# Optimization experiments

Hardware: AMD Instinct MI355X
Metric: run time of the kernel (lower is better)

## Reference

```python
import jax, jax.numpy as jnp
import numpy as np

F_DIM = 1024
HEAD = 16
MLP_H = 4096
EPS = 1e-5


def _layernorm(x, g, b):
    mu = jnp.mean(x, axis=-1, keepdims=True)
    var = jnp.var(x, axis=-1, keepdims=True)
    return (x - mu) * jax.lax.rsqrt(var + EPS) * g + b


def setup_inputs() -> dict:
    key = jax.random.key(0)
    ks = jax.random.split(key, 16)
    B, T, F = 2, 2048, F_DIM
    s = 1.0 / np.sqrt(F)
    sm = 1.0 / np.sqrt(MLP_H)
    return {
        "x": jax.random.normal(ks[0], (B, T, F), jnp.float32),
        "ln1_g": jnp.ones((F,), jnp.float32),
        "ln1_b": jnp.zeros((F,), jnp.float32),
        "Wq": jax.random.normal(ks[1], (F, F), jnp.float32) * s,
        "bq": jnp.zeros((F,), jnp.float32),
        "Wk": jax.random.normal(ks[2], (F, F), jnp.float32) * s,
        "bk": jnp.zeros((F,), jnp.float32),
        "Wv": jax.random.normal(ks[3], (F, F), jnp.float32) * s,
        "bv": jnp.zeros((F,), jnp.float32),
        "Wo": jax.random.normal(ks[4], (F, F), jnp.float32) * s,
        "bo": jnp.zeros((F,), jnp.float32),
        "ln2_g": jnp.ones((F,), jnp.float32),
        "ln2_b": jnp.zeros((F,), jnp.float32),
        "W1": jax.random.normal(ks[5], (F, MLP_H), jnp.float32) * s,
        "b1": jnp.zeros((MLP_H,), jnp.float32),
        "W2": jax.random.normal(ks[6], (MLP_H, F), jnp.float32) * sm,
        "b2": jnp.zeros((F,), jnp.float32),
    }


def reference(x, ln1_g, ln1_b, Wq, bq, Wk, bk, Wv, bv, Wo, bo, ln2_g, ln2_b, W1, b1, W2, b2):
    B, T, F = x.shape
    H, Dh = HEAD, F // HEAD
    sqrt_d = jnp.asarray(F, x.dtype) ** 0.5  # NOTE: scale by sqrt(features), as in source

    h = _layernorm(x, ln1_g, ln1_b)
    Q = (h @ Wq + bq).reshape(B, T, H, Dh).transpose(0, 2, 1, 3)  # bhtd
    K = (h @ Wk + bk).reshape(B, T, H, Dh).transpose(0, 2, 1, 3)
    V = (h @ Wv + bv).reshape(B, T, H, Dh).transpose(0, 2, 1, 3)

    scores = jnp.einsum('bhif,bhjf->bhij', Q, K) / sqrt_d
    attn_map = jax.nn.softmax(scores, axis=-1)
    attn = jnp.einsum('bhij,bhjf->bihf', attn_map, V)  # [B,T,H,Dh]
    attn_out = attn.reshape(B, T, F) @ Wo + bo
    out = attn_out + x

    h2 = _layernorm(out, ln2_g, ln2_b)
    mlp = jax.nn.gelu(jax.nn.gelu(h2 @ W1 + b1, approximate=False) @ W2 + b2, approximate=False)
    return mlp + out
```

## Files before the change

### kernel.cpp

```cpp
#include <hip/hip_runtime.h>
#include <hip/hip_bf16.h>
#include <math.h>
#include <stdint.h>

typedef __attribute__((ext_vector_type(8))) __bf16 bf16x8;
typedef __attribute__((ext_vector_type(4))) float f32x4;

#define F_DIM 1024
#define MLP_HD 4096
#define HEADS 16
#define DH 64
#define B_SZ 2
#define T_SZ 2048
#define NROWS 4096
#define QKV_N 3072
#define LN_EPS 1e-5f

__device__ __forceinline__ void gload16(const void* g, void* l) {
    __builtin_amdgcn_global_load_lds(
        (const __attribute__((address_space(1))) uint32_t*)(uintptr_t)g,
        (__attribute__((address_space(3))) uint32_t*)(uintptr_t)l,
        16, 0, 0);
}

__global__ void transpose_cast(const float* __restrict__ in,
                               __hip_bfloat16* __restrict__ out,
                               int R, int C) {
    __shared__ float tile[32][33];
    int c0 = blockIdx.x * 32, r0 = blockIdx.y * 32;
    int tx = threadIdx.x, ty = threadIdx.y;
    #pragma unroll
    for (int i = 0; i < 32; i += 8)
        tile[ty + i][tx] = in[(size_t)(r0 + ty + i) * C + c0 + tx];
    __syncthreads();
    #pragma unroll
    for (int i = 0; i < 32; i += 8)
        out[(size_t)(c0 + ty + i) * R + r0 + tx] = __float2bfloat16(tile[tx][ty + i]);
}

__global__ void transpose_v(const __hip_bfloat16* __restrict__ QKV,
                            __hip_bfloat16* __restrict__ VT) {
    __shared__ __hip_bfloat16 tile[32][33];
    int dblk = blockIdx.y & 1, bh = blockIdx.y >> 1;
    int b = bh >> 4, h = bh & 15;
    int t0 = blockIdx.x * 32, d0 = dblk * 32;
    int tx = threadIdx.x, ty = threadIdx.y;
    #pragma unroll
    for (int i = 0; i < 32; i += 8)
        tile[ty + i][tx] = QKV[(size_t)(b * T_SZ + t0 + ty + i) * QKV_N + 2048 + h * DH + d0 + tx];
    __syncthreads();
    #pragma unroll
    for (int i = 0; i < 32; i += 8)
        VT[(size_t)(bh * DH + d0 + ty + i) * T_SZ + t0 + tx] = tile[tx][ty + i];
}

__global__ void concat_bias(const float* __restrict__ a, const float* __restrict__ b,
                            const float* __restrict__ c, float* __restrict__ o) {
    int i = blockIdx.x * 256 + threadIdx.x;
    o[i] = i < 1024 ? a[i] : (i < 2048 ? b[i - 1024] : c[i - 2048]);
}

__global__ void layernorm_bf16_k(const float* __restrict__ x,
                                 const float* __restrict__ g,
                                 const float* __restrict__ b,
                                 __hip_bfloat16* __restrict__ out) {
    int row = blockIdx.x;
    const float* xr = x + (size_t)row * F_DIM;
    int t = threadIdx.x;
    float4 v = ((const float4*)xr)[t];
    float s  = v.x + v.y + v.z + v.w;
    float s2 = v.x * v.x + v.y * v.y + v.z * v.z + v.w * v.w;
    #pragma unroll
    for (int off = 32; off >= 1; off >>= 1) {
        s  += __shfl_down(s, off);
        s2 += __shfl_down(s2, off);
    }
    __shared__ float rs_[4], rs2_[4];
    int wave = t >> 6, lane = t & 63;
    if (lane == 0) { rs_[wave] = s; rs2_[wave] = s2; }
    __syncthreads();
    float S  = rs_[0] + rs_[1] + rs_[2] + rs_[3];
    float S2 = rs2_[0] + rs2_[1] + rs2_[2] + rs2_[3];
    float mu  = S * (1.0f / F_DIM);
    float var = S2 * (1.0f / F_DIM) - mu * mu;
    float rstd = rsqrtf(var + LN_EPS);
    float4 gv = ((const float4*)g)[t];
    float4 bv = ((const float4*)b)[t];
    __hip_bfloat16* orow = out + (size_t)row * F_DIM;
    orow[t * 4 + 0] = __float2bfloat16((v.x - mu) * rstd * gv.x + bv.x);
    orow[t * 4 + 1] = __float2bfloat16((v.y - mu) * rstd * gv.y + bv.y);
    orow[t * 4 + 2] = __float2bfloat16((v.z - mu) * rstd * gv.z + bv.z);
    orow[t * 4 + 3] = __float2bfloat16((v.w - mu) * rstd * gv.w + bv.w);
}

__device__ __forceinline__ float gelu_exact(float x) {
    return 0.5f * x * (1.0f + erff(x * 0.70710678f));
}

#define LA_PTR(BUF, H) ((__hip_bfloat16*)(SMEM + ((BUF) * 2 + (H)) * 16384))
#define LB_PTR(BUF, H) ((__hip_bfloat16*)(SMEM + 65536 + ((BUF) * 2 + (H)) * 16384))

#define MFMA_QUAD(AF, BF, MB, NB)                                              \
  do {                                                                         \
    __builtin_amdgcn_s_barrier();                                              \
    asm volatile("s_waitcnt lgkmcnt(0)" ::: "memory");                         \
    __builtin_amdgcn_sched_barrier(0);                                         \
    __builtin_amdgcn_s_setprio(1);                                             \
    _Pragma("unroll") for (int ks = 0; ks < 2; ++ks)                           \
      _Pragma("unroll") for (int a_ = 0; a_ < 4; ++a_)                         \
        _Pragma("unroll") for (int b_ = 0; b_ < 2; ++b_)                       \
          acc[(MB) + a_][(NB) + b_] = __builtin_amdgcn_mfma_f32_16x16x32_bf16( \
              AF[a_][ks], BF[b_][ks], acc[(MB) + a_][(NB) + b_], 0, 0, 0);     \
    __builtin_amdgcn_s_setprio(0);                                             \
  } while (0)

#define LDA_FRAGS(DST, BUF, MQ)                                                \
  do {                                                                         \
    _Pragma("unroll") for (int a_ = 0; a_ < 4; ++a_)                           \
      _Pragma("unroll") for (int ks = 0; ks < 2; ++ks) {                       \
        int row_ = (MQ) * 64 + a_ * 16 + fr;                                   \
        int byt_ = row_ * 128 + ((ks * 64 + fq * 16) ^ ((row_ & 7) << 4));     \
        DST[a_][ks] = *(const bf16x8*)((const char*)LA_PTR(BUF, wm) + byt_);   \
      }                                                                        \
  } while (0)

#define LDB_FRAGS(DST, BUF, NQ)                                                \
  do {                                                                         \
    _Pragma("unroll") for (int b_ = 0; b_ < 2; ++b_)                           \
      _Pragma("unroll") for (int ks = 0; ks < 2; ++ks) {                       \
        int row_ = (wn & 1) * 64 + ((NQ) * 2 + b_) * 16 + fr;                  \
        int byt_ = row_ * 128 + ((ks * 64 + fq * 16) ^ ((row_ & 7) << 4));     \
        DST[b_][ks] = *(const bf16x8*)((const char*)LB_PTR(BUF, hb) + byt_);   \
      }                                                                        \
  } while (0)

#define STAGE_A(BUF, H, KT_)                                                   \
  do {                                                                         \
    _Pragma("unroll") for (int q_ = 0; q_ < 2; ++q_)                           \
      gload16(A + (size_t)(m0 + (H) * 128 + srow[q_]) * K +                    \
                  (k00 + (KT_) * 64 + scol[q_]),                               \
              LA_PTR(BUF, H) + q_ * 4096 + t * 8);                             \
  } while (0)

#define STAGE_B(BUF, H, KT_)                                                   \
  do {                                                                         \
    _Pragma("unroll") for (int q_ = 0; q_ < 2; ++q_)                           \
      gload16(BT + (size_t)(n0 + (H) * 128 + srow[q_]) * K +                   \
                   (k00 + (KT_) * 64 + scol[q_]),                              \
              LB_PTR(BUF, H) + q_ * 4096 + t * 8);                             \
  } while (0)

template <int EPI, int KLEN>
__global__ __launch_bounds__(512, 2) void gemm256(
    const __hip_bfloat16* __restrict__ A,
    const __hip_bfloat16* __restrict__ BT,
    const float* __restrict__ bias,
    void* __restrict__ Cout,
    int M, int N, int K) {
    __shared__ __align__(16) char SMEM[131072];

    int t = threadIdx.x;
    int w = t >> 6, lane = t & 63;
    int wm = w >> 2, wn = w & 3;
    int fr = lane & 15, fq = lane >> 4;
    int hb = wn >> 1;

    int gx = gridDim.x, gy = gridDim.y, gz = gridDim.z;
    int bid = blockIdx.x + gx * (blockIdx.y + gy * blockIdx.z);
    int nwg = gx * gy * gz;
    int qch = nwg >> 3;
    int logical = (bid & 7) * qch + (bid >> 3);
    int pp = gy * gz;
    int bx = logical / pp;
    int rr = logical % pp;
    int by = rr / gz;
    int bz = rr % gz;

    int m0 = by * 256, n0 = bx * 256;
    int k00 = bz * KLEN;

    int srow[2], scol[2];
    #pragma unroll
    for (int q = 0; q < 2; ++q) {
        int u = q * 8192 + t * 16;
        u ^= ((u >> 7) & 7) << 4;
        srow[q] = u >> 7;
        scol[q] = (u & 127) >> 1;
    }

    f32x4 acc[8][4] = {};
    bf16x8 aflo[4][2], afhi[4][2], bflo[2][2], bfhi[2][2];
    constexpr int KT = KLEN >> 6;

    STAGE_A(0, 0, 0); STAGE_A(0, 1, 0); STAGE_B(0, 0, 0); STAGE_B(0, 1, 0);
    STAGE_A(1, 0, 1); STAGE_A(1, 1, 1);
    asm volatile("s_waitcnt vmcnt(4)" ::: "memory");
    __builtin_amdgcn_s_barrier();

    for (int i = 0;; ++i) {
        int k1 = 2 * i + 1;
        int nx2 = (2 * i + 2) & (KT - 1), nx3 = (2 * i + 3) & (KT - 1);
        LDA_FRAGS(aflo, 0, 0);
        LDB_FRAGS(bflo, 0, 0);
        STAGE_B(1, 0, k1);
        MFMA_QUAD(aflo, bflo, 0, 0);
        __builtin_amdgcn_s_barrier();
        LDA_FRAGS(afhi, 0, 1);
        STAGE_B(1, 1, k1);
        MFMA_QUAD(afhi, bflo, 4, 0);
        __builtin_amdgcn_s_barrier();
        LDB_FRAGS(bfhi, 0, 1);
        STAGE_A(0, 0, nx2);
        MFMA_QUAD(afhi, bfhi, 4, 2);
        __builtin_amdgcn_s_barrier();
        STAGE_A(0, 1, nx2);
        MFMA_QUAD(aflo, bfhi, 0, 2);
        asm volatile("s_waitcnt vmcnt(4)" ::: "memory");
        __builtin_amdgcn_s_barrier();
        LDA_FRAGS(aflo, 1, 0);
        LDB_FRAGS(bflo, 1, 0);
        STAGE_B(0, 0, nx2);
        MFMA_QUAD(aflo, bflo, 0, 0);
        __builtin_amdgcn_s_barrier();
        LDA_FRAGS(afhi, 1, 1);
        STAGE_B(0, 1, nx2);
        MFMA_QUAD(afhi, bflo, 4, 0);
        __builtin_amdgcn_s_barrier();
        LDB_FRAGS(bfhi, 1, 1);
        STAGE_A(1, 0, nx3);
        MFMA_QUAD(afhi, bfhi, 4, 2);
        __builtin_amdgcn_s_barrier();
        STAGE_A(1, 1, nx3);
        MFMA_QUAD(aflo, bfhi, 0, 2);
        asm volatile("s_waitcnt vmcnt(4)" ::: "memory");
        __builtin_amdgcn_s_barrier();
        if (2 * i + 2 >= KT) break;
    }

    asm volatile("s_waitcnt vmcnt(0)" ::: "memory");
    __builtin_amdgcn_s_barrier();

    #pragma unroll
    for (int ni = 0; ni < 4; ++ni) {
        int col = wn * 64 + ni * 16 + fr;
        float bv = (EPI == 4) ? 0.f : bias[n0 + col];
        #pragma unroll
        for (int mi = 0; mi < 8; ++mi) {
            #pragma unroll
            for (int j = 0; j < 4; ++j) {
                int row = wm * 128 + mi * 16 + fq * 4 + j;
                float v = acc[mi][ni][j] + bv;
                if constexpr (EPI == 2) v = gelu_exact(v);
                int byt = row * 512 + ((col * 2) ^ ((row & 7) << 4));
                *(__hip_bfloat16*)(SMEM + byt) = __float2bfloat16(v);
            }
        }
    }
    __builtin_amdgcn_s_barrier();

    __hip_bfloat16* outc = (__hip_bfloat16*)Cout;
    if constexpr (EPI == 4) outc += (size_t)bz * ((size_t)M * N);
    #pragma unroll
    for (int p = 0; p < 16; ++p) {
        int row = p * 16 + (t >> 5);
        int chunk = t & 31;
        int byt = row * 512 + ((chunk * 16) ^ ((row & 7) << 4));
        bf16x8 vv = *(const bf16x8*)(SMEM + byt);
        *(bf16x8*)&outc[(size_t)(m0 + row) * N + n0 + chunk * 8] = vv;
    }
}

__global__ __launch_bounds__(256) void mlp2_reduce(
    const __hip_bfloat16* __restrict__ P,
    const float* __restrict__ b2,
    const float* __restrict__ res,
    float* __restrict__ out) {
    int i = (blockIdx.x * 256 + threadIdx.x) * 8;
    float s[8] = {};
    #pragma unroll
    for (int sk = 0; sk < 4; ++sk) {
        bf16x8 v = *(const bf16x8*)&P[(size_t)sk * ((size_t)NROWS * F_DIM) + i];
        #pragma unroll
        for (int u = 0; u < 8; ++u) s[u] += (float)v[u];
    }
    int col = i & (F_DIM - 1);
    #pragma unroll
    for (int u = 0; u < 8; ++u)
        out[i + u] = gelu_exact(s[u] + b2[col + u]) + res[i + u];
}

template <int EPI, int BM>
__global__ __launch_bounds__(256) void gemm_bt(
    const __hip_bfloat16* __restrict__ A,
    const __hip_bfloat16* __restrict__ BT,
    const float* __restrict__ bias,
    const float* __restrict__ res,
    void* __restrict__ Cout,
    int M, int N, int K) {
    constexpr int MI = BM / 32;
    constexpr int AQ = BM / 64;
    __shared__ __hip_bfloat16 As[2][BM * 32];
    __shared__ __hip_bfloat16 Bs[2][128 * 32];

    int t = threadIdx.x;
    int m0 = blockIdx.y * BM, n0 = blockIdx.x * 128;
    int w = t >> 6, lane = t & 63;
    int wr = (w >> 1) * (BM / 2), wc = (w & 1) * 64;
    int fr = lane & 15, fq = lane >> 4;

    int scol = (lane & 3) * 8;
    int srowA = w * (BM / 4) + (lane >> 2);
    int srowB = w * 32 + (lane >> 2);
    const __hip_bfloat16* Ag = A  + (size_t)(m0 + srowA) * K + scol;
    const __hip_bfloat16* Bg = BT + (size_t)(n0 + srowB) * K + scol;
    int lofsA = w * (BM / 4) * 32 + lane * 8;
    int lofsB = w * 1024 + lane * 8;

    f32x4 acc[MI][4] = {};
    int KT = K >> 5;
    int cur = 0;

    #pragma unroll
    for (int q = 0; q < AQ; ++q)
        gload16(Ag + (size_t)q * 16 * K, &As[0][lofsA + q * 512]);
    #pragma unroll
    for (int q = 0; q < 2; ++q)
        gload16(Bg + (size_t)q * 16 * K, &Bs[0][lofsB + q * 512]);
    __syncthreads();

    for (int kt = 0; kt < KT; ++kt) {
        if (kt + 1 < KT) {
            const __hip_bfloat16* An = Ag + (size_t)(kt + 1) * 32;
            const __hip_bfloat16* Bn = Bg + (size_t)(kt + 1) * 32;
            #pragma unroll
            for (int q = 0; q < AQ; ++q)
                gload16(An + (size_t)q * 16 * K, &As[cur ^ 1][lofsA + q * 512]);
            #pragma unroll
            for (int q = 0; q < 2; ++q)
                gload16(Bn + (size_t)q * 16 * K, &Bs[cur ^ 1][lofsB + q * 512]);
        }
        bf16x8 af[MI], bfr[4];
        #pragma unroll
        for (int mi = 0; mi < MI; ++mi)
            af[mi] = *(const bf16x8*)&As[cur][(wr + mi * 16 + fr) * 32 + fq * 8];
        #pragma unroll
        for (int ni = 0; ni < 4; ++ni)
            bfr[ni] = *(const bf16x8*)&Bs[cur][(wc + ni * 16 + fr) * 32 + fq * 8];
        #pragma unroll
        for (int mi = 0; mi < MI; ++mi)
            #pragma unroll
            for (int ni = 0; ni < 4; ++ni)
                acc[mi][ni] = __builtin_amdgcn_mfma_f32_16x16x32_bf16(
                    af[mi], bfr[ni], acc[mi][ni], 0, 0, 0);
        __syncthreads();
        cur ^= 1;
    }

    #pragma unroll
    for (int ni = 0; ni < 4; ++ni) {
        int col = n0 + wc + ni * 16 + fr;
        float bv = bias[col];
        #pragma unroll
        for (int mi = 0; mi < MI; ++mi) {
            #pragma unroll
            for (int j = 0; j < 4; ++j) {
                int row = m0 + wr + mi * 16 + fq * 4 + j;
                size_t idx = (size_t)row * N + col;
                float v = acc[mi][ni][j] + bv;
                if constexpr (EPI == 1) {
                    ((float*)Cout)[idx] = v + res[idx];
                } else {
                    ((__hip_bfloat16*)Cout)[idx] = __float2bfloat16(v);
                }
            }
        }
    }
}

__global__ __launch_bounds__(256) void attn_mfma(
    const __hip_bfloat16* __restrict__ QKV,
    const __hip_bfloat16* __restrict__ VT,
    __hip_bfloat16* __restrict__ O) {
    __shared__ __hip_bfloat16 Kt[2][64][72];
    __shared__ __hip_bfloat16 Vt[2][64][72];
    __shared__ __hip_bfloat16 Ps[4][32][72];

    int blk = blockIdx.x;
    int qb = blk & 15;
    int bh = blk >> 4;
    int b = bh >> 4, h = bh & 15;
    int t = threadIdx.x;
    int w = t >> 6, lane = t & 63;
    int fr = lane & 15, fq = lane >> 4;

    bf16x8 qf[2][2];
    #pragma unroll
    for (int mt = 0; mt < 2; ++mt)
        #pragma unroll
        for (int ks = 0; ks < 2; ++ks) {
            int qrow = qb * 128 + w * 32 + mt * 16 + fr;
            const __hip_bfloat16* src =
                QKV + (size_t)(b * T_SZ + qrow) * QKV_N + h * DH + ks * 32 + fq * 8;
            bf16x8 v = *(const bf16x8*)src;
            #pragma unroll
            for (int u = 0; u < 8; ++u) v[u] = (__bf16)((float)v[u] * 0.03125f);
            qf[mt][ks] = v;
        }

    f32x4 oacc[2][4] = {};
    float lsum[2][4] = {};

    int sr = t >> 2;
    int sc = (t & 3) * 16;
    const __hip_bfloat16* Kg = QKV + (size_t)(b * T_SZ + sr) * QKV_N + F_DIM + h * DH + sc;
    const __hip_bfloat16* Vg = VT + (size_t)(bh * DH + sr) * T_SZ + sc;

    bf16x8 kr0, kr1, vr0, vr1;
    {
        kr0 = *(const bf16x8*)Kg;       kr1 = *(const bf16x8*)(Kg + 8);
        vr0 = *(const bf16x8*)Vg;       vr1 = *(const bf16x8*)(Vg + 8);
        *(bf16x8*)&Kt[0][sr][sc]     = kr0;
        *(bf16x8*)&Kt[0][sr][sc + 8] = kr1;
        *(bf16x8*)&Vt[0][sr][sc]     = vr0;
        *(bf16x8*)&Vt[0][sr][sc + 8] = vr1;
    }
    __syncthreads();

    int cur = 0;
    for (int j0 = 0; j0 < T_SZ; j0 += 64) {
        bool more = (j0 + 64 < T_SZ);
        if (more) {
            const __hip_bfloat16* kg = Kg + (size_t)(j0 + 64) * QKV_N;
            kr0 = *(const bf16x8*)kg;  kr1 = *(const bf16x8*)(kg + 8);
            const __hip_bfloat16* vg = Vg + (j0 + 64);
            vr0 = *(const bf16x8*)vg;  vr1 = *(const bf16x8*)(vg + 8);
        }

        f32x4 sacc[2][4] = {};
        __builtin_amdgcn_s_setprio(1);
        #pragma unroll
        for (int ks = 0; ks < 2; ++ks) {
            bf16x8 kf[4];
            #pragma unroll
            for (int nt = 0; nt < 4; ++nt)
                kf[nt] = *(const bf16x8*)&Kt[cur][nt * 16 + fr][ks * 32 + fq * 8];
            #pragma unroll
            for (int mt = 0; mt < 2; ++mt)
                #pragma unroll
                for (int nt = 0; nt < 4; ++nt)
                    sacc[mt][nt] = __builtin_amdgcn_mfma_f32_16x16x32_bf16(
                        qf[mt][ks], kf[nt], sacc[mt][nt], 0, 0, 0);
        }
        __builtin_amdgcn_s_setprio(0);

        bf16x8 vb[2][4];
        #pragma unroll
        for (int ks = 0; ks < 2; ++ks)
            #pragma unroll
            for (int nt = 0; nt < 4; ++nt)
                vb[ks][nt] = *(const bf16x8*)&Vt[cur][nt * 16 + fr][ks * 32 + fq * 8];

        #pragma unroll
        for (int mt = 0; mt < 2; ++mt) {
            #pragma unroll
            for (int r = 0; r < 4; ++r) {
                #pragma unroll
                for (int nt = 0; nt < 4; ++nt) {
                    float p = __expf(sacc[mt][nt][r]);
                    lsum[mt][r] += p;
                    Ps[w][mt * 16 + fq * 4 + r][nt * 16 + fr] = __float2bfloat16(p);
                }
            }
        }

        asm volatile("s_waitcnt lgkmcnt(0)" ::: "memory");
        __builtin_amdgcn_sched_barrier(0);

        __builtin_amdgcn_s_setprio(1);
        #pragma unroll
        for (int ks = 0; ks < 2; ++ks) {
            bf16x8 ap[2];
            #pragma unroll
            for (int mt = 0; mt < 2; ++mt)
                ap[mt] = *(const bf16x8*)&Ps[w][mt * 16 + fr][ks * 32 + fq * 8];
            #pragma unroll
            for (int nt = 0; nt < 4; ++nt) {
                #pragma unroll
                for (int mt = 0; mt < 2; ++mt)
                    oacc[mt][nt] = __builtin_amdgcn_mfma_f32_16x16x32_bf16(
                        ap[mt], vb[ks][nt], oacc[mt][nt], 0, 0, 0);
            }
        }
        __builtin_amdgcn_s_setprio(0);

        if (more) {
            *(bf16x8*)&Kt[cur ^ 1][sr][sc]     = kr0;
            *(bf16x8*)&Kt[cur ^ 1][sr][sc + 8] = kr1;
            *(bf16x8*)&Vt[cur ^ 1][sr][sc]     = vr0;
            *(bf16x8*)&Vt[cur ^ 1][sr][sc + 8] = vr1;
        }
        __syncthreads();
        cur ^= 1;
    }

    #pragma unroll
    for (int mt = 0; mt < 2; ++mt) {
        #pragma unroll
        for (int r = 0; r < 4; ++r) {
            float l = lsum[mt][r];
            #pragma unroll
            for (int d = 1; d < 16; d <<= 1) l += __shfl_xor(l, d);
            float rl = 1.0f / l;
            int row = qb * 128 + w * 32 + mt * 16 + fq * 4 + r;
            #pragma unroll
            for (int nt = 0; nt < 4; ++nt)
                O[(size_t)(b * T_SZ + row) * F_DIM + h * DH + nt * 16 + fr] =
                    __float2bfloat16(oacc[mt][nt][r] * rl);
        }
    }
}

extern "C" void kernel_launch(void* const* d_in, const int* in_sizes, int n_in,
                              void* d_out, int out_size, void* d_ws, size_t ws_size,
                              hipStream_t stream) {
    const float* x     = (const float*)d_in[0];
    const float* ln1_g = (const float*)d_in[1];
    const float* ln1_b = (const float*)d_in[2];
    const float* Wq    = (const float*)d_in[3];
    const float* bq    = (const float*)d_in[4];
    const float* Wk    = (const float*)d_in[5];
    const float* bk    = (const float*)d_in[6];
    const float* Wv    = (const float*)d_in[7];
    const float* bv    = (const float*)d_in[8];
    const float* Wo    = (const float*)d_in[9];
    const float* bo    = (const float*)d_in[10];
    const float* ln2_g = (const float*)d_in[11];
    const float* ln2_b = (const float*)d_in[12];
    const float* W1    = (const float*)d_in[13];
    const float* b1    = (const float*)d_in[14];
    const float* W2    = (const float*)d_in[15];
    const float* b2    = (const float*)d_in[16];
    float* outp = (float*)d_out;

    char* ws = (char*)d_ws;
    size_t off = 0;
    auto alloc = [&](size_t bytes) {
        void* p = ws + off;
        off += (bytes + 255) & ~(size_t)255;
        return p;
    };
    __hip_bfloat16* WqkvT = (__hip_bfloat16*)alloc((size_t)QKV_N * 1024 * 2);
    __hip_bfloat16* WoT   = (__hip_bfloat16*)alloc((size_t)1024 * 1024 * 2);
    __hip_bfloat16* W1T   = (__hip_bfloat16*)alloc((size_t)4096 * 1024 * 2);
    __hip_bfloat16* W2T   = (__hip_bfloat16*)alloc((size_t)4096 * 1024 * 2);
    float*          qkvb  = (float*)alloc((size_t)QKV_N * 4);
    __hip_bfloat16* h1    = (__hip_bfloat16*)alloc((size_t)NROWS * F_DIM * 2);
    __hip_bfloat16* QKVb  = (__hip_bfloat16*)alloc((size_t)NROWS * QKV_N * 2);
    __hip_bfloat16* VTb   = (__hip_bfloat16*)alloc((size_t)32 * DH * T_SZ * 2);
    __hip_bfloat16* attnO = (__hip_bfloat16*)alloc((size_t)NROWS * F_DIM * 2);
    float*          outb  = (float*)alloc((size_t)NROWS * F_DIM * 4);
    __hip_bfloat16* h2    = (__hip_bfloat16*)alloc((size_t)NROWS * F_DIM * 2);
    __hip_bfloat16* mlp1  = (__hip_bfloat16*)alloc((size_t)NROWS * MLP_HD * 2);
    __hip_bfloat16* mlp2P = h1;
    (void)ws_size; (void)in_sizes; (void)n_in; (void)out_size;

    dim3 tb(32, 8);
    transpose_cast<<<dim3(32, 32), tb, 0, stream>>>(Wq, WqkvT,               1024, 1024);
    transpose_cast<<<dim3(32, 32), tb, 0, stream>>>(Wk, WqkvT + 1024 * 1024, 1024, 1024);
    transpose_cast<<<dim3(32, 32), tb, 0, stream>>>(Wv, WqkvT + 2048 * 1024, 1024, 1024);
    transpose_cast<<<dim3(32, 32), tb, 0, stream>>>(Wo, WoT, 1024, 1024);
    transpose_cast<<<dim3(128, 32), tb, 0, stream>>>(W1, W1T, 1024, 4096);
    transpose_cast<<<dim3(32, 128), tb, 0, stream>>>(W2, W2T, 4096, 1024);
    concat_bias<<<12, 256, 0, stream>>>(bq, bk, bv, qkvb);

    layernorm_bf16_k<<<NROWS, 256, 0, stream>>>(x, ln1_g, ln1_b, h1);

    gemm256<0, 1024><<<dim3(QKV_N / 256, NROWS / 256, 1), 512, 0, stream>>>(
        h1, WqkvT, qkvb, QKVb, NROWS, QKV_N, 1024);

    transpose_v<<<dim3(T_SZ / 32, 64), tb, 0, stream>>>(QKVb, VTb);

    attn_mfma<<<512, 256, 0, stream>>>(QKVb, VTb, attnO);

    gemm_bt<1, 64><<<dim3(8, 64), 256, 0, stream>>>(attnO, WoT, bo, x, outb, NROWS, 1024, 1024);

    layernorm_bf16_k<<<NROWS, 256, 0, stream>>>(outb, ln2_g, ln2_b, h2);

    gemm256<2, 1024><<<dim3(MLP_HD / 256, NROWS / 256, 1), 512, 0, stream>>>(
        h2, W1T, b1, mlp1, NROWS, MLP_HD, 1024);

    gemm256<4, 1024><<<dim3(F_DIM / 256, NROWS / 256, 4), 512, 0, stream>>>(
        mlp1, W2T, nullptr, mlp2P, NROWS, F_DIM, MLP_HD);

    mlp2_reduce<<<2048, 256, 0, stream>>>(mlp2P, b2, outb, outp);
}
```

Baseline: 264.3 us.

## Software-pipeline attention so next tile's QK^T overlaps current softmax and PV

Restructures the attention inner loop so each step computes the QK^T scores for the next key tile while doing exp and PV for the current one, ping-ponging two score register sets. K is now prefetched three tiles ahead and V two tiles ahead. The loop is manually unrolled by two. The change also pads the LDS rows from 72 to 76 elements and sets launch_bounds occupancy to 2. The aim is to hide MFMA and LDS latency behind the exp work, at the cost of more live registers, which the occupancy hint may cause to spill.

New measurement: 264.0 us. About the same (-0.1%).

```diff
diff --git a/kernel.cpp b/kernel.cpp
--- a/kernel.cpp
+++ b/kernel.cpp
@@ -377,13 +377,77 @@
     }
 }
 
-__global__ __launch_bounds__(256) void attn_mfma(
+#define NT 32
+
+#define QK_TILE(SN, BUF)                                                       \
+  do {                                                                         \
+    bf16x8 kf0[4], kf1[4];                                                     \
+    _Pragma("unroll") for (int nt = 0; nt < 4; ++nt) {                         \
+        kf0[nt] = *(const bf16x8*)&Kt[BUF][nt * 16 + fr][fq * 8];              \
+        kf1[nt] = *(const bf16x8*)&Kt[BUF][nt * 16 + fr][32 + fq * 8];         \
+    }                                                                          \
+    _Pragma("unroll") for (int mt = 0; mt < 2; ++mt)                           \
+        _Pragma("unroll") for (int nt = 0; nt < 4; ++nt) {                     \
+            f32x4 zz = {0.f, 0.f, 0.f, 0.f};                                   \
+            f32x4 s0_ = __builtin_amdgcn_mfma_f32_16x16x32_bf16(               \
+                qf[mt][0], kf0[nt], zz, 0, 0, 0);                              \
+            SN[mt][nt] = __builtin_amdgcn_mfma_f32_16x16x32_bf16(              \
+                qf[mt][1], kf1[nt], s0_, 0, 0, 0);                             \
+        }                                                                      \
+  } while (0)
+
+#define ATTN_STEP(SP, SN, I)                                                   \
+  do {                                                                         \
+    int cw = (I) & 1, nw = cw ^ 1;                                             \
+    if ((I) + 2 < NT) {                                                        \
+        *(bf16x8*)&Kt[cw][sr][sc]     = kr0;                                   \
+        *(bf16x8*)&Kt[cw][sr][sc + 8] = kr1;                                   \
+    }                                                                          \
+    if ((I) + 1 < NT) {                                                        \
+        *(bf16x8*)&Vt[nw][sr][sc]     = vr0;                                   \
+        *(bf16x8*)&Vt[nw][sr][sc + 8] = vr1;                                   \
+    }                                                                          \
+    if ((I) + 3 < NT) {                                                        \
+        const __hip_bfloat16* kg_ = Kg + (size_t)(((I) + 3) * 64) * QKV_N;     \
+        kr0 = *(const bf16x8*)kg_; kr1 = *(const bf16x8*)(kg_ + 8);            \
+    }                                                                          \
+    if ((I) + 2 < NT) {                                                        \
+        const __hip_bfloat16* vg_ = Vg + ((I) + 2) * 64;                       \
+        vr0 = *(const bf16x8*)vg_; vr1 = *(const bf16x8*)(vg_ + 8);            \
+    }                                                                          \
+    if ((I) + 1 < NT) { QK_TILE(SN, nw); }                                     \
+    _Pragma("unroll") for (int mt = 0; mt < 2; ++mt)                           \
+        _Pragma("unroll") for (int r = 0; r < 4; ++r)                          \
+            _Pragma("unroll") for (int nt = 0; nt < 4; ++nt) {                 \
+                float p_ = __expf(SP[mt][nt][r]);                              \
+                lsum[mt][r] += p_;                                             \
+                Ps[w][mt * 16 + fq * 4 + r][nt * 16 + fr] = __float2bfloat16(p_); \
+            }                                                                  \
+    asm volatile("s_waitcnt lgkmcnt(0)" ::: "memory");                         \
+    __builtin_amdgcn_sched_barrier(0);                                         \
+    __builtin_amdgcn_s_setprio(1);                                             \
+    _Pragma("unroll") for (int ks = 0; ks < 2; ++ks) {                         \
+        bf16x8 ap[2];                                                          \
+        _Pragma("unroll") for (int mt = 0; mt < 2; ++mt)                       \
+            ap[mt] = *(const bf16x8*)&Ps[w][mt * 16 + fr][ks * 32 + fq * 8];   \
+        _Pragma("unroll") for (int nt = 0; nt < 4; ++nt) {                     \
+            bf16x8 vbv = *(const bf16x8*)&Vt[cw][nt * 16 + fr][ks * 32 + fq * 8]; \
+            _Pragma("unroll") for (int mt = 0; mt < 2; ++mt)                   \
+                oacc[mt][nt] = __builtin_amdgcn_mfma_f32_16x16x32_bf16(        \
+                    ap[mt], vbv, oacc[mt][nt], 0, 0, 0);                       \
+        }                                                                      \
+    }                                                                          \
+    __builtin_amdgcn_s_setprio(0);                                             \
+    __syncthreads();                                                           \
+  } while (0)
+
+__global__ __launch_bounds__(256, 2) void attn_mfma(
     const __hip_bfloat16* __restrict__ QKV,
     const __hip_bfloat16* __restrict__ VT,
     __hip_bfloat16* __restrict__ O) {
-    __shared__ __hip_bfloat16 Kt[2][64][72];
-    __shared__ __hip_bfloat16 Vt[2][64][72];
-    __shared__ __hip_bfloat16 Ps[4][32][72];
+    __shared__ __hip_bfloat16 Kt[2][64][76];
+    __shared__ __hip_bfloat16 Vt[2][64][76];
+    __shared__ __hip_bfloat16 Ps[4][32][76];
 
     int blk = blockIdx.x;
     int qb = blk & 15;
@@ -409,6 +473,7 @@
 
     f32x4 oacc[2][4] = {};
     float lsum[2][4] = {};
+    f32x4 sA[2][4], sB[2][4];
 
     int sr = t >> 2;
     int sc = (t & 3) * 16;
@@ -416,91 +481,33 @@
     const __hip_bfloat16* Vg = VT + (size_t)(bh * DH + sr) * T_SZ + sc;
 
     bf16x8 kr0, kr1, vr0, vr1;
+
+    kr0 = *(const bf16x8*)Kg;  kr1 = *(const bf16x8*)(Kg + 8);
+    *(bf16x8*)&Kt[0][sr][sc]     = kr0;
+    *(bf16x8*)&Kt[0][sr][sc + 8] = kr1;
     {
-        kr0 = *(const bf16x8*)Kg;       kr1 = *(const bf16x8*)(Kg + 8);
-        vr0 = *(const bf16x8*)Vg;       vr1 = *(const bf16x8*)(Vg + 8);
-        *(bf16x8*)&Kt[0][sr][sc]     = kr0;
-        *(bf16x8*)&Kt[0][sr][sc + 8] = kr1;
-        *(bf16x8*)&Vt[0][sr][sc]     = vr0;
-        *(bf16x8*)&Vt[0][sr][sc + 8] = vr1;
-    }
+        const __hip_bfloat16* kg_ = Kg + (size_t)64 * QKV_N;
+        kr0 = *(const bf16x8*)kg_; kr1 = *(const bf16x8*)(kg_ + 8);
+    }
+    vr0 = *(const bf16x8*)Vg;  vr1 = *(const bf16x8*)(Vg + 8);
     __syncthreads();
-
-    int cur = 0;
-    for (int j0 = 0; j0 < T_SZ; j0 += 64) {
-        bool more = (j0 + 64 < T_SZ);
-        if (more) {
-            const __hip_bfloat16* kg = Kg + (size_t)(j0 + 64) * QKV_N;
-            kr0 = *(const bf16x8*)kg;  kr1 = *(const bf16x8*)(kg + 8);
-            const __hip_bfloat16* vg = Vg + (j0 + 64);
-            vr0 = *(const bf16x8*)vg;  vr1 = *(const bf16x8*)(vg + 8);
-        }
-
-        f32x4 sacc[2][4] = {};
-        __builtin_amdgcn_s_setprio(1);
-        #pragma unroll
-        for (int ks = 0; ks < 2; ++ks) {
-            bf16x8 kf[4];
-            #pragma unroll
-            for (int nt = 0; nt < 4; ++nt)
-                kf[nt] = *(const bf16x8*)&Kt[cur][nt * 16 + fr][ks * 32 + fq * 8];
-            #pragma unroll
-            for (int mt = 0; mt < 2; ++mt)
-                #pragma unroll
-                for (int nt = 0; nt < 4; ++nt)
-                    sacc[mt][nt] = __builtin_amdgcn_mfma_f32_16x16x32_bf16(
-                        qf[mt][ks], kf[nt], sacc[mt][nt], 0, 0, 0);
-        }
-        __builtin_amdgcn_s_setprio(0);
-
-        bf16x8 vb[2][4];
-        #pragma unroll
-        for (int ks = 0; ks < 2; ++ks)
-            #pragma unroll
-            for (int nt = 0; nt < 4; ++nt)
-                vb[ks][nt] = *(const bf16x8*)&Vt[cur][nt * 16 + fr][ks * 32 + fq * 8];
-
-        #pragma unroll
-        for (int mt = 0; mt < 2; ++mt) {
-            #pragma unroll
-            for (int r = 0; r < 4; ++r) {
-                #pragma unroll
-                for (int nt = 0; nt < 4; ++nt) {
-                    float p = __expf(sacc[mt][nt][r]);
-                    lsum[mt][r] += p;
-                    Ps[w][mt * 16 + fq * 4 + r][nt * 16 + fr] = __float2bfloat16(p);
-                }
-            }
-        }
-
-        asm volatile("s_waitcnt lgkmcnt(0)" ::: "memory");
-        __builtin_amdgcn_sched_barrier(0);
-
-        __builtin_amdgcn_s_setprio(1);
-        #pragma unroll
-        for (int ks = 0; ks < 2; ++ks) {
-            bf16x8 ap[2];
-            #pragma unroll
-            for (int mt = 0; mt < 2; ++mt)
-                ap[mt] = *(const bf16x8*)&Ps[w][mt * 16 + fr][ks * 32 + fq * 8];
-            #pragma unroll
-            for (int nt = 0; nt < 4; ++nt) {
-                #pragma unroll
-                for (int mt = 0; mt < 2; ++mt)
-                    oacc[mt][nt] = __builtin_amdgcn_mfma_f32_16x16x32_bf16(
-                        ap[mt], vb[ks][nt], oacc[mt][nt], 0, 0, 0);
-            }
-        }
-        __builtin_amdgcn_s_setprio(0);
-
-        if (more) {
-            *(bf16x8*)&Kt[cur ^ 1][sr][sc]     = kr0;
-            *(bf16x8*)&Kt[cur ^ 1][sr][sc + 8] = kr1;
-            *(bf16x8*)&Vt[cur ^ 1][sr][sc]     = vr0;
-            *(bf16x8*)&Vt[cur ^ 1][sr][sc + 8] = vr1;
-        }
-        __syncthreads();
-        cur ^= 1;
+    QK_TILE(sA, 0);
+    *(bf16x8*)&Kt[1][sr][sc]     = kr0;
+    *(bf16x8*)&Kt[1][sr][sc + 8] = kr1;
+    *(bf16x8*)&Vt[0][sr][sc]     = vr0;
+    *(bf16x8*)&Vt[0][sr][sc + 8] = vr1;
+    {
+        const __hip_bfloat16* kg_ = Kg + (size_t)128 * QKV_N;
+        kr0 = *(const bf16x8*)kg_; kr1 = *(const bf16x8*)(kg_ + 8);
+        const __hip_bfloat16* vg_ = Vg + 64;
+        vr0 = *(const bf16x8*)vg_; vr1 = *(const bf16x8*)(vg_ + 8);
+    }
+    __syncthreads();
+
+    #pragma unroll 1
+    for (int i = 0; i < NT; i += 2) {
+        ATTN_STEP(sA, sB, i);
+        ATTN_STEP(sB, sA, i + 1);
     }
 
     #pragma unroll
```

## Restructure attention KV loop to 32-key tiles with two-ahead prefetch

Applied to the files above, without the earlier changes.

Shrinks the attention key/value tile from 64 to 32 keys and reshapes the shared-memory buffers and padding to match. Global loads now run two tiles ahead through registers while the next LDS buffer is written at the top of each iteration. It also adds launch bounds asking for 4 blocks per CU and remaps block indices so blocks that share K/V are spread differently. The aim is lower register and LDS pressure for higher occupancy and better latency hiding, at the cost of twice as many loop iterations and barriers.

Result: no change. 262.7 us (-0.6%).

```diff
diff --git a/kernel.cpp b/kernel.cpp
--- a/kernel.cpp
+++ b/kernel.cpp
@@ -377,15 +377,19 @@
     }
 }
 
-__global__ __launch_bounds__(256) void attn_mfma(
+#define KVB 32
+#define NT2 (T_SZ / KVB)
+
+__global__ __launch_bounds__(256, 4) void attn_mfma(
     const __hip_bfloat16* __restrict__ QKV,
     const __hip_bfloat16* __restrict__ VT,
     __hip_bfloat16* __restrict__ O) {
-    __shared__ __hip_bfloat16 Kt[2][64][72];
-    __shared__ __hip_bfloat16 Vt[2][64][72];
-    __shared__ __hip_bfloat16 Ps[4][32][72];
-
-    int blk = blockIdx.x;
+    __shared__ __hip_bfloat16 Kt[2][KVB][72];
+    __shared__ __hip_bfloat16 Vt[2][DH][44];
+    __shared__ __hip_bfloat16 Ps[4][32][40];
+
+    int hw = blockIdx.x;
+    int blk = (hw & 7) * 64 + (hw >> 3);
     int qb = blk & 15;
     int bh = blk >> 4;
     int b = bh >> 4, h = bh & 15;
@@ -410,97 +414,86 @@
     f32x4 oacc[2][4] = {};
     float lsum[2][4] = {};
 
-    int sr = t >> 2;
-    int sc = (t & 3) * 16;
-    const __hip_bfloat16* Kg = QKV + (size_t)(b * T_SZ + sr) * QKV_N + F_DIM + h * DH + sc;
-    const __hip_bfloat16* Vg = VT + (size_t)(bh * DH + sr) * T_SZ + sc;
-
-    bf16x8 kr0, kr1, vr0, vr1;
-    {
-        kr0 = *(const bf16x8*)Kg;       kr1 = *(const bf16x8*)(Kg + 8);
-        vr0 = *(const bf16x8*)Vg;       vr1 = *(const bf16x8*)(Vg + 8);
-        *(bf16x8*)&Kt[0][sr][sc]     = kr0;
-        *(bf16x8*)&Kt[0][sr][sc + 8] = kr1;
-        *(bf16x8*)&Vt[0][sr][sc]     = vr0;
-        *(bf16x8*)&Vt[0][sr][sc + 8] = vr1;
-    }
+    int krow = t >> 3, kcol = (t & 7) * 8;
+    int vrow = t >> 2, vcol = (t & 3) * 8;
+    const __hip_bfloat16* Kg = QKV + (size_t)(b * T_SZ + krow) * QKV_N + F_DIM + h * DH + kcol;
+    const __hip_bfloat16* Vg = VT + (size_t)(bh * DH + vrow) * T_SZ + vcol;
+
+    bf16x8 kr, vr;
+    kr = *(const bf16x8*)Kg;
+    vr = *(const bf16x8*)Vg;
+    *(bf16x8*)&Kt[0][krow][kcol] = kr;
+    *(bf16x8*)&Vt[0][vrow][vcol] = vr;
+    kr = *(const bf16x8*)(Kg + (size_t)KVB * QKV_N);
+    vr = *(const bf16x8*)(Vg + KVB);
     __syncthreads();
 
-    int cur = 0;
-    for (int j0 = 0; j0 < T_SZ; j0 += 64) {
-        bool more = (j0 + 64 < T_SZ);
-        if (more) {
-            const __hip_bfloat16* kg = Kg + (size_t)(j0 + 64) * QKV_N;
-            kr0 = *(const bf16x8*)kg;  kr1 = *(const bf16x8*)(kg + 8);
-            const __hip_bfloat16* vg = Vg + (j0 + 64);
-            vr0 = *(const bf16x8*)vg;  vr1 = *(const bf16x8*)(vg + 8);
-        }
-
-        f32x4 sacc[2][4] = {};
+    #pragma unroll 2
+    for (int i = 0; i < NT2; ++i) {
+        int cur = i & 1;
+        if (i + 1 < NT2) {
+            *(bf16x8*)&Kt[cur ^ 1][krow][kcol] = kr;
+            *(bf16x8*)&Vt[cur ^ 1][vrow][vcol] = vr;
+        }
+        if (i + 2 < NT2) {
+            kr = *(const bf16x8*)(Kg + (size_t)(i + 2) * KVB * QKV_N);
+            vr = *(const bf16x8*)(Vg + (i + 2) * KVB);
+        }
+
+        f32x4 sacc[2][2];
         __builtin_amdgcn_s_setprio(1);
-        #pragma unroll
-        for (int ks = 0; ks < 2; ++ks) {
-            bf16x8 kf[4];
-            #pragma unroll
-            for (int nt = 0; nt < 4; ++nt)
-                kf[nt] = *(const bf16x8*)&Kt[cur][nt * 16 + fr][ks * 32 + fq * 8];
+        {
+            bf16x8 kf[2][2];
+            #pragma unroll
+            for (int nt = 0; nt < 2; ++nt)
+                #pragma unroll
+                for (int ks = 0; ks < 2; ++ks)
+                    kf[nt][ks] = *(const bf16x8*)&Kt[cur][nt * 16 + fr][ks * 32 + fq * 8];
             #pragma unroll
             for (int mt = 0; mt < 2; ++mt)
                 #pragma unroll
-                for (int nt = 0; nt < 4; ++nt)
+                for (int nt = 0; nt < 2; ++nt) {
+                    f32x4 zz = {0.f, 0.f, 0.f, 0.f};
+                    f32x4 s0 = __builtin_amdgcn_mfma_f32_16x16x32_bf16(
+                        qf[mt][0], kf[nt][0], zz, 0, 0, 0);
                     sacc[mt][nt] = __builtin_amdgcn_mfma_f32_16x16x32_bf16(
-                        qf[mt][ks], kf[nt], sacc[mt][nt], 0, 0, 0);
+                        qf[mt][1], kf[nt][1], s0, 0, 0, 0);
+                }
         }
         __builtin_amdgcn_s_setprio(0);
 
-        bf16x8 vb[2][4];
-        #pragma unroll
-        for (int ks = 0; ks < 2; ++ks)
-            #pragma unroll
-            for (int nt = 0; nt < 4; ++nt)
-                vb[ks][nt] = *(const bf16x8*)&Vt[cur][nt * 16 + fr][ks * 32 + fq * 8];
-
-        #pragma unroll
-        for (int mt = 0; mt < 2; ++mt) {
-            #pragma unroll
-            for (int r = 0; r < 4; ++r) {
+        #pragma unroll
+        for (int mt = 0; mt < 2; ++mt)
+            #pragma unroll
+            for (int r = 0; r < 4; ++r)
                 #pragma unroll
-                for (int nt = 0; nt < 4; ++nt) {
+                for (int nt = 0; nt < 2; ++nt) {
                     float p = __expf(sacc[mt][nt][r]);
                     lsum[mt][r] += p;
                     Ps[w][mt * 16 + fq * 4 + r][nt * 16 + fr] = __float2bfloat16(p);
                 }
-            }
-        }
 
         asm volatile("s_waitcnt lgkmcnt(0)" ::: "memory");
         __builtin_amdgcn_sched_barrier(0);
 
         __builtin_amdgcn_s_setprio(1);
-        #pragma unroll
-        for (int ks = 0; ks < 2; ++ks) {
+        {
             bf16x8 ap[2];
             #pragma unroll
             for (int mt = 0; mt < 2; ++mt)
-                ap[mt] = *(const bf16x8*)&Ps[w][mt * 16 + fr][ks * 32 + fq * 8];
-            #pragma unroll
-            for (int nt = 0; nt < 4; ++nt) {
+                ap[mt] = *(const bf16x8*)&Ps[w][mt * 16 + fr][fq * 8];
+            #pragma unroll
+            for (int nd = 0; nd < 4; ++nd) {
+                bf16x8 vbv = *(const bf16x8*)&Vt[cur][nd * 16 + fr][fq * 8];
                 #pragma unroll
                 for (int mt = 0; mt < 2; ++mt)
-                    oacc[mt][nt] = __builtin_amdgcn_mfma_f32_16x16x32_bf16(
-                        ap[mt], vb[ks][nt], oacc[mt][nt], 0, 0, 0);
+                    oacc[mt][nd] = __builtin_amdgcn_mfma_f32_16x16x32_bf16(
+                        ap[mt], vbv, oacc[mt][nd], 0, 0, 0);
             }
         }
         __builtin_amdgcn_s_setprio(0);
 
-        if (more) {
-            *(bf16x8*)&Kt[cur ^ 1][sr][sc]     = kr0;
-            *(bf16x8*)&Kt[cur ^ 1][sr][sc + 8] = kr1;
-            *(bf16x8*)&Vt[cur ^ 1][sr][sc]     = vr0;
-            *(bf16x8*)&Vt[cur ^ 1][sr][sc + 8] = vr1;
-        }
         __syncthreads();
-        cur ^= 1;
     }
 
     #pragma unroll
```
